# Performance work log

Hardware: AMD Instinct MI355X
Metric: run time of the kernel (lower is better)

## Reference

```python
import jax, jax.numpy as jnp
import numpy as np

# Architecture dims (from setArch args)
B, IN = 256, 1024          # batch, inputSize
E, H1, S = 32, 1024, 512   # numStateEnsembles, stateHiddenLayerSize, stateEnsembleOutputSize
H2, F = 512, 64            # featureHiddenLayerSize, numStateFeatures
NO, HO, OF = 16, 512, 1    # numOutputEnsembles, outputEnsembleHiddenLayerSize, outputEnsembleFeatures
T = E * F                  # thalamusSpaceSize
TIN = IN + T               # totalInputSize


def setup_inputs() -> dict:
    key = jax.random.key(0)
    ks = jax.random.split(key, 14)
    sc = 0.02
    f32 = jnp.float32
    return {
        "inputs": jax.random.normal(ks[0], (B, IN), f32),
        # stacked state-ensemble params: Linear(TIN,H1) -> Softplus -> Linear(H1,S)
        "sw1": jax.random.normal(ks[1], (E, TIN, H1), f32) * sc,
        "sb1": jax.random.normal(ks[2], (E, H1), f32) * sc,
        "sw2": jax.random.normal(ks[3], (E, H1, S), f32) * sc,
        "sb2": jax.random.normal(ks[4], (E, S), f32) * sc,
        # stacked feature-ensemble params: Linear(S,H2) -> ReLU -> Linear(H2,F)
        "fw1": jax.random.normal(ks[5], (E, S, H2), f32) * sc,
        "fb1": jax.random.normal(ks[6], (E, H2), f32) * sc,
        "fw2": jax.random.normal(ks[7], (E, H2, F), f32) * sc,
        "fb2": jax.random.normal(ks[8], (E, F), f32) * sc,
        # stacked output-ensemble params: Linear(S+1,HO) -> ReLU -> Linear(HO,OF)
        "ow1": jax.random.normal(ks[9], (NO, S + 1, HO), f32) * sc,
        "ob1": jax.random.normal(ks[10], (NO, HO), f32) * sc,
        "ow2": jax.random.normal(ks[11], (NO, HO, OF), f32) * sc,
        "ob2": jax.random.normal(ks[12], (NO, OF), f32) * sc,
        "action": 1,
        "context": 3,
        "num_iterations": 4,
    }


def reference(inputs, sw1, sb1, sw2, sb2, fw1, fb1, fw2, fb2,
              ow1, ob1, ow2, ob2, action, context, num_iterations):
    b = inputs.shape[0]
    # resetThalamus: savedThalamusFeatures = zeros(E*F)
    thal = jnp.zeros((b, T), inputs.dtype)
    state = None
    for _ in range(num_iterations):
        # leInput = cat(thalamusFeatures, inputs)  -> [B, TIN]
        x = jnp.concatenate([thal, inputs], axis=-1)
        # all E state ensembles batched: Linear -> Softplus -> Linear
        h = jax.nn.softplus(jnp.einsum('bi,eih->beh', x, sw1) + sb1)   # [B,E,H1]
        state = jnp.einsum('beh,ehs->bes', h, sw2) + sb2               # [B,E,S]
        # all E feature ensembles batched: Linear -> ReLU -> Linear
        g = jax.nn.relu(jnp.einsum('bes,esh->beh', state, fw1) + fb1)  # [B,E,H2]
        feat = jnp.einsum('beh,ehf->bef', g, fw2) + fb2                # [B,E,F]
        # thalamusFeatures = concatenate(computedFeatures)
        thal = feat.reshape(b, T)
    # output ensemble for `context` on cat([action], stateValues[context])
    sc_state = state[:, context, :]                                    # [B,S]
    a = jnp.full((b, 1), action, inputs.dtype)
    y = jnp.concatenate([a, sc_state], axis=-1)                        # [B,S+1]
    z = jax.nn.relu(y @ ow1[context] + ob1[context])                   # [B,HO]
    reward = z @ ow2[context] + ob2[context]                           # [B,OF]
    return reward
```

## Files before the change

### kernel.cpp

```cpp
#include <hip/hip_runtime.h>
#include <hip/hip_bf16.h>

#define B_SZ 256
#define IN_  1024
#define E_   32
#define H1_  1024
#define S_   512
#define H2_  512
#define F_   64
#define T_   2048
#define TIN_ 3072
#define NO_  16
#define HO_  512

typedef __attribute__((ext_vector_type(8))) short bf16x8;
typedef __attribute__((ext_vector_type(4))) float f32x4;

__device__ __forceinline__ unsigned short f2bf(float f) {
    unsigned u = __builtin_bit_cast(unsigned, f);
    u += 0x7fffu + ((u >> 16) & 1u);
    return (unsigned short)(u >> 16);
}
__device__ __forceinline__ float bf2f(unsigned short h) {
    return __builtin_bit_cast(float, ((unsigned)h) << 16);
}
__device__ __forceinline__ float softplusf(float x) {
    return fmaxf(x, 0.0f) + log1pf(expf(-fabsf(x)));
}
__device__ __forceinline__ void gload_lds16(const void* g, void* l) {
    __builtin_amdgcn_global_load_lds(
        (const __attribute__((address_space(1))) unsigned int*)g,
        (__attribute__((address_space(3))) unsigned int*)l,
        16, 0, 0);
}

__global__ __launch_bounds__(256) void cvt_t64(const float* __restrict__ in,
                                               unsigned short* __restrict__ out,
                                               int K, int N) {
    __shared__ float tile[64][65];
    const size_t eoff = (size_t)blockIdx.z * K * N;
    const float* ip = in + eoff;
    unsigned short* op = out + eoff;
    const int k0 = blockIdx.x * 64, n0 = blockIdx.y * 64;
    const int t = threadIdx.x;
    const int lr = t >> 4;
    const int lc = (t & 15) << 2;
    #pragma unroll
    for (int i = 0; i < 4; ++i) {
        const float4 v = *(const float4*)&ip[(size_t)(k0 + lr + 16 * i) * N + n0 + lc];
        float* dst = &tile[lr + 16 * i][lc];
        dst[0] = v.x; dst[1] = v.y; dst[2] = v.z; dst[3] = v.w;
    }
    __syncthreads();
    #pragma unroll
    for (int i = 0; i < 4; ++i) {
        const int n = (t >> 4) + 16 * i;
        const int k = (t & 15) << 2;
        ushort4 o;
        o.x = f2bf(tile[k][n]); o.y = f2bf(tile[k + 1][n]);
        o.z = f2bf(tile[k + 2][n]); o.w = f2bf(tile[k + 3][n]);
        *(ushort4*)&op[(size_t)(n0 + n) * K + k0 + k] = o;
    }
}

__global__ void x_init(const float* __restrict__ inp, unsigned short* __restrict__ x) {
    const int i = blockIdx.x * 256 + threadIdx.x;
    const int b = i / (IN_ / 4), c = (i % (IN_ / 4)) * 4;
    const float4 v = *(const float4*)&inp[(size_t)b * IN_ + c];
    ushort4 o;
    o.x = f2bf(v.x); o.y = f2bf(v.y); o.z = f2bf(v.z); o.w = f2bf(v.w);
    *(ushort4*)&x[(size_t)b * TIN_ + T_ + c] = o;
}

template<int BM, int BN, int TPB, int ACT, int ADD_BASE, int OUTM>
__global__ __launch_bounds__(TPB) void gemm_k(
    const unsigned short* __restrict__ A, int lda, long strideAe,
    int kOff, int K,
    const unsigned short* __restrict__ W, int ldw, long strideWe,
    const float* __restrict__ bias,
    const float* __restrict__ baseBuf,
    void* __restrict__ out, void* __restrict__ out2,
    int ldc, long strideOe, int N)
{
    constexpr int NW = TPB / 64;
    constexpr int WM_ = 2, WN_ = NW / 2;
    constexpr int MI = BM / (16 * WM_), NI = BN / (16 * WN_);
    constexpr int AL = (BM * 4) / TPB, BL = (BN * 4) / TPB;
    __shared__ unsigned short As0[BM * 32], Bs0[BN * 32];
    __shared__ unsigned short As1[BM * 32], Bs1[BN * 32];
    const int e = blockIdx.z;
    const int m0 = blockIdx.x * BM;
    const int n0 = blockIdx.y * BN;
    const int tid = threadIdx.x;
    const int wid = tid >> 6;
    const int lane = tid & 63;
    const int wm = wid / WN_, wn = wid % WN_;
    const unsigned short* Ae = A + (size_t)e * strideAe + (size_t)m0 * lda + kOff;
    const unsigned short* We = W + (size_t)e * strideWe + (size_t)n0 * ldw + kOff;

    f32x4 acc[MI][NI];
    #pragma unroll
    for (int i = 0; i < MI; ++i)
        #pragma unroll
        for (int j = 0; j < NI; ++j) {
            f32x4 z = {0.f, 0.f, 0.f, 0.f};
            acc[i][j] = z;
        }
    const int lr = lane & 15;
    const int lk = (lane >> 4) << 3;

    auto stage = [&](unsigned short* Asb, unsigned short* Bsb, int kt) {
        const int kk = kt * 32;
        #pragma unroll
        for (int p = 0; p < AL; ++p) {
            const int seg = p * TPB + tid;
            const int r = seg >> 2, cc = (seg & 3) << 3;
            gload_lds16(Ae + (size_t)r * lda + kk + cc, Asb + ((size_t)(p * TPB + wid * 64)) * 8);
        }
        #pragma unroll
        for (int p = 0; p < BL; ++p) {
            const int seg = p * TPB + tid;
            const int r = seg >> 2, cc = (seg & 3) << 3;
            gload_lds16(We + (size_t)r * ldw + kk + cc, Bsb + ((size_t)(p * TPB + wid * 64)) * 8);
        }
    };
    auto compute = [&](const unsigned short* Asb, const unsigned short* Bsb) {
        bf16x8 af2[MI], bfv[NI];
        #pragma unroll
        for (int mi = 0; mi < MI; ++mi)
            af2[mi] = *(const bf16x8*)&Asb[(wm * MI * 16 + mi * 16 + lr) * 32 + lk];
        #pragma unroll
        for (int ni = 0; ni < NI; ++ni)
            bfv[ni] = *(const bf16x8*)&Bsb[(wn * NI * 16 + ni * 16 + lr) * 32 + lk];
        #pragma unroll
        for (int mi = 0; mi < MI; ++mi)
            #pragma unroll
            for (int ni = 0; ni < NI; ++ni)
                acc[mi][ni] = __builtin_amdgcn_mfma_f32_16x16x32_bf16(
                    af2[mi], bfv[ni], acc[mi][ni], 0, 0, 0);
    };

    const int nt = K / 32;
    stage(As0, Bs0, 0);
    __syncthreads();
    for (int t = 0; t < nt; t += 2) {
        stage(As1, Bs1, t + 1);
        compute(As0, Bs0);
        __syncthreads();
        if (t + 2 < nt) stage(As0, Bs0, t + 2);
        compute(As1, Bs1);
        __syncthreads();
    }

    const int lg = lane >> 4;
    #pragma unroll
    for (int ni = 0; ni < NI; ++ni) {
        const int col = n0 + wn * NI * 16 + ni * 16 + lr;
        const float bv = bias ? bias[(size_t)e * N + col] : 0.0f;
        #pragma unroll
        for (int mi = 0; mi < MI; ++mi) {
            #pragma unroll
            for (int r = 0; r < 4; ++r) {
                const int row = m0 + wm * MI * 16 + mi * 16 + lg * 4 + r;
                float v = acc[mi][ni][r] + bv;
                if constexpr (ADD_BASE) v += baseBuf[((size_t)e * B_SZ + row) * H1_ + col];
                if constexpr (ACT == 1) v = softplusf(v);
                if constexpr (ACT == 2) v = fmaxf(v, 0.0f);
                const size_t oidx = (size_t)e * strideOe + (size_t)row * ldc + col;
                if constexpr (OUTM == 2) {
                    ((float*)out)[oidx] = v;
                    ((unsigned short*)out2)[oidx] = f2bf(softplusf(v));
                } else {
                    ((unsigned short*)out)[oidx] = f2bf(v);
                }
            }
        }
    }
    (void)out2;
}

__global__ __launch_bounds__(512) void head_z(const unsigned short* __restrict__ state,
                                              const float* __restrict__ ow1,
                                              const float* __restrict__ ob1,
                                              const int* __restrict__ actp,
                                              const int* __restrict__ ctxp,
                                              float* __restrict__ z) {
    __shared__ float ys[16][516];
    const int ctx = *ctxp;
    const float act = (float)(*actp);
    const int b0 = blockIdx.x * 16;
    const int t = threadIdx.x;
    for (int bb = 0; bb < 16; ++bb)
        ys[bb][1 + t] = bf2f(state[((size_t)(ctx * B_SZ + b0 + bb)) * S_ + t]);
    if (t < 16) ys[t][0] = act;
    __syncthreads();
    const float* w = ow1 + (size_t)ctx * (S_ + 1) * HO_;
    float acc[16];
    #pragma unroll
    for (int bb = 0; bb < 16; ++bb) acc[bb] = 0.0f;
    for (int k = 0; k < S_ + 1; ++k) {
        const float wv = w[(size_t)k * HO_ + t];
        #pragma unroll
        for (int bb = 0; bb < 16; ++bb) acc[bb] += ys[bb][k] * wv;
    }
    const float b1 = ob1[ctx * HO_ + t];
    for (int bb = 0; bb < 16; ++bb)
        z[(size_t)(b0 + bb) * HO_ + t] = fmaxf(acc[bb] + b1, 0.0f);
}

__global__ void head_r(const float* __restrict__ z, const float* __restrict__ ow2,
                       const float* __restrict__ ob2, const int* __restrict__ ctxp,
                       float* __restrict__ out) {
    const int ctx = *ctxp;
    const int b = blockIdx.x;
    const int t = threadIdx.x;
    const float* w = ow2 + (size_t)ctx * HO_;
    float s = 0.0f;
    for (int h = t; h < HO_; h += 64) s += z[(size_t)b * HO_ + h] * w[h];
    #pragma unroll
    for (int off = 32; off; off >>= 1) s += __shfl_down(s, off);
    if (t == 0) out[b] = s + ob2[ctx];
}

extern "C" void kernel_launch(void* const* d_in, const int* in_sizes, int n_in,
                              void* d_out, int out_size, void* d_ws, size_t ws_size,
                              hipStream_t stream) {
    (void)in_sizes; (void)n_in; (void)out_size; (void)ws_size;
    const float* inputs = (const float*)d_in[0];
    const float* sw1 = (const float*)d_in[1];
    const float* sb1 = (const float*)d_in[2];
    const float* sw2 = (const float*)d_in[3];
    const float* sb2 = (const float*)d_in[4];
    const float* fw1 = (const float*)d_in[5];
    const float* fb1 = (const float*)d_in[6];
    const float* fw2 = (const float*)d_in[7];
    const float* fb2 = (const float*)d_in[8];
    const float* ow1 = (const float*)d_in[9];
    const float* ob1 = (const float*)d_in[10];
    const float* ow2 = (const float*)d_in[11];
    const float* ob2 = (const float*)d_in[12];
    const int* actp = (const int*)d_in[13];
    const int* ctxp = (const int*)d_in[14];

    char* p = (char*)d_ws;
    unsigned short* w1t = (unsigned short*)p; p += (size_t)E_ * H1_ * TIN_ * 2;
    unsigned short* w2t = (unsigned short*)p; p += (size_t)E_ * S_ * H1_ * 2;
    unsigned short* f1t = (unsigned short*)p; p += (size_t)E_ * H2_ * S_ * 2;
    unsigned short* f2t = (unsigned short*)p; p += (size_t)E_ * F_ * H2_ * 2;
    unsigned short* xbf = (unsigned short*)p; p += (size_t)B_SZ * TIN_ * 2;
    float* base = (float*)p;                  p += (size_t)E_ * B_SZ * H1_ * 4;
    unsigned short* hbf = (unsigned short*)p; p += (size_t)E_ * B_SZ * H1_ * 2;
    unsigned short* stbf = (unsigned short*)p; p += (size_t)E_ * B_SZ * S_ * 2;
    unsigned short* gbf = (unsigned short*)p; p += (size_t)E_ * B_SZ * H2_ * 2;
    float* zbuf = (float*)p;                  p += (size_t)B_SZ * HO_ * 4;

    cvt_t64<<<dim3(TIN_ / 64, H1_ / 64, E_), 256, 0, stream>>>(sw1, w1t, TIN_, H1_);
    cvt_t64<<<dim3(H1_ / 64, S_ / 64, E_),  256, 0, stream>>>(sw2, w2t, H1_, S_);
    cvt_t64<<<dim3(S_ / 64, H2_ / 64, E_),  256, 0, stream>>>(fw1, f1t, S_, H2_);
    cvt_t64<<<dim3(H2_ / 64, F_ / 64, E_),  256, 0, stream>>>(fw2, f2t, H2_, F_);
    x_init<<<(B_SZ * IN_ / 4) / 256, 256, 0, stream>>>(inputs, xbf);

    gemm_k<128, 64, 256, 0, 0, 2><<<dim3(2, H1_ / 64, E_), 256, 0, stream>>>(
        xbf, TIN_, 0L, T_, IN_, w1t, TIN_, (long)H1_ * TIN_, sb1, nullptr,
        base, hbf, H1_, (long)B_SZ * H1_, H1_);

    for (int it = 0; it < 4; ++it) {
        if (it > 0) {
            gemm_k<128, 64, 256, 1, 1, 0><<<dim3(2, H1_ / 64, E_), 256, 0, stream>>>(
                xbf, TIN_, 0L, 0, T_, w1t, TIN_, (long)H1_ * TIN_, nullptr, base,
                hbf, nullptr, H1_, (long)B_SZ * H1_, H1_);
        }
        gemm_k<64, 64, 256, 0, 0, 0><<<dim3(4, S_ / 64, E_), 256, 0, stream>>>(
            hbf, H1_, (long)B_SZ * H1_, 0, H1_, w2t, H1_, (long)S_ * H1_, sb2, nullptr,
            stbf, nullptr, S_, (long)B_SZ * S_, S_);
        if (it < 3) {
            gemm_k<64, 64, 256, 2, 0, 0><<<dim3(4, H2_ / 64, E_), 256, 0, stream>>>(
                stbf, S_, (long)B_SZ * S_, 0, S_, f1t, S_, (long)H2_ * S_, fb1, nullptr,
                gbf, nullptr, H2_, (long)B_SZ * H2_, H2_);
            gemm_k<64, 64, 256, 0, 0, 0><<<dim3(4, 1, E_), 256, 0, stream>>>(
                gbf, H2_, (long)B_SZ * H2_, 0, H2_, f2t, H2_, (long)F_ * H2_, fb2, nullptr,
                xbf, nullptr, TIN_, 64L, F_);
        }
    }
    head_z<<<B_SZ / 16, 512, 0, stream>>>(stbf, ow1, ob1, actp, ctxp, zbuf);
    head_r<<<B_SZ, 64, 0, stream>>>(zbuf, ow2, ob2, ctxp, (float*)d_out);
}
```

Before: 880.9 us.

## Enlarge GEMM tiles, remap blocks M-major across ensembles, store base in bf16

Makes the warp layout a template parameter and moves the big first-layer GEMMs to 128x128 tiles with 512 threads. It also moves the second-layer and feature GEMMs to 128x64 tiles. A flat 1D grid ordered so that the two M-halves of the same weight tile are scheduled far apart (bid>>8) is meant to spread ensembles across CUs and keep the wave count even at 512 blocks. The precomputed input-part base activation is now stored in bf16 instead of fp32, halving its write and re-read traffic. The bf16 base adds rounding error to the pre-softplus sum.

```diff
diff --git a/kernel.cpp b/kernel.cpp
--- a/kernel.cpp
+++ b/kernel.cpp
@@ -72,29 +72,37 @@
     *(ushort4*)&x[(size_t)b * TIN_ + T_ + c] = o;
 }
 
-template<int BM, int BN, int TPB, int ACT, int ADD_BASE, int OUTM>
+template<int BM, int BN, int TPB, int WMT, int WNT, int ACT, int ADD_BASE, int OUTM, bool PAIRED>
 __global__ __launch_bounds__(TPB) void gemm_k(
     const unsigned short* __restrict__ A, int lda, long strideAe,
     int kOff, int K,
     const unsigned short* __restrict__ W, int ldw, long strideWe,
     const float* __restrict__ bias,
-    const float* __restrict__ baseBuf,
+    const unsigned short* __restrict__ baseBuf,
     void* __restrict__ out, void* __restrict__ out2,
     int ldc, long strideOe, int N)
 {
-    constexpr int NW = TPB / 64;
-    constexpr int WM_ = 2, WN_ = NW / 2;
-    constexpr int MI = BM / (16 * WM_), NI = BN / (16 * WN_);
+    constexpr int MI = BM / (16 * WMT), NI = BN / (16 * WNT);
     constexpr int AL = (BM * 4) / TPB, BL = (BN * 4) / TPB;
     __shared__ unsigned short As0[BM * 32], Bs0[BN * 32];
     __shared__ unsigned short As1[BM * 32], Bs1[BN * 32];
-    const int e = blockIdx.z;
-    const int m0 = blockIdx.x * BM;
-    const int n0 = blockIdx.y * BN;
+
+    int e, m0, n0;
+    if constexpr (PAIRED) {
+        const int bid = blockIdx.x;
+        const int NBn = N / BN;
+        m0 = (bid >> 8) * BM;
+        const int rem = bid & 255;
+        n0 = (rem % NBn) * BN;
+        e  = rem / NBn;
+    } else {
+        e = blockIdx.z; m0 = blockIdx.x * BM; n0 = blockIdx.y * BN;
+    }
+
     const int tid = threadIdx.x;
     const int wid = tid >> 6;
     const int lane = tid & 63;
-    const int wm = wid / WN_, wn = wid % WN_;
+    const int wm = wid / WNT, wn = wid % WNT;
     const unsigned short* Ae = A + (size_t)e * strideAe + (size_t)m0 * lda + kOff;
     const unsigned short* We = W + (size_t)e * strideWe + (size_t)n0 * ldw + kOff;
 
@@ -163,12 +171,12 @@
             for (int r = 0; r < 4; ++r) {
                 const int row = m0 + wm * MI * 16 + mi * 16 + lg * 4 + r;
                 float v = acc[mi][ni][r] + bv;
-                if constexpr (ADD_BASE) v += baseBuf[((size_t)e * B_SZ + row) * H1_ + col];
+                if constexpr (ADD_BASE) v += bf2f(baseBuf[((size_t)e * B_SZ + row) * H1_ + col]);
                 if constexpr (ACT == 1) v = softplusf(v);
                 if constexpr (ACT == 2) v = fmaxf(v, 0.0f);
                 const size_t oidx = (size_t)e * strideOe + (size_t)row * ldc + col;
                 if constexpr (OUTM == 2) {
-                    ((float*)out)[oidx] = v;
+                    ((unsigned short*)out)[oidx] = f2bf(v);
                     ((unsigned short*)out2)[oidx] = f2bf(softplusf(v));
                 } else {
                     ((unsigned short*)out)[oidx] = f2bf(v);
@@ -248,7 +256,7 @@
     unsigned short* f1t = (unsigned short*)p; p += (size_t)E_ * H2_ * S_ * 2;
     unsigned short* f2t = (unsigned short*)p; p += (size_t)E_ * F_ * H2_ * 2;
     unsigned short* xbf = (unsigned short*)p; p += (size_t)B_SZ * TIN_ * 2;
-    float* base = (float*)p;                  p += (size_t)E_ * B_SZ * H1_ * 4;
+    unsigned short* base = (unsigned short*)p; p += (size_t)E_ * B_SZ * H1_ * 2;
     unsigned short* hbf = (unsigned short*)p; p += (size_t)E_ * B_SZ * H1_ * 2;
     unsigned short* stbf = (unsigned short*)p; p += (size_t)E_ * B_SZ * S_ * 2;
     unsigned short* gbf = (unsigned short*)p; p += (size_t)E_ * B_SZ * H2_ * 2;
@@ -260,24 +268,24 @@
     cvt_t64<<<dim3(H2_ / 64, F_ / 64, E_),  256, 0, stream>>>(fw2, f2t, H2_, F_);
     x_init<<<(B_SZ * IN_ / 4) / 256, 256, 0, stream>>>(inputs, xbf);
 
-    gemm_k<128, 64, 256, 0, 0, 2><<<dim3(2, H1_ / 64, E_), 256, 0, stream>>>(
+    gemm_k<128, 128, 512, 2, 4, 0, 0, 2, true><<<dim3(512), 512, 0, stream>>>(
         xbf, TIN_, 0L, T_, IN_, w1t, TIN_, (long)H1_ * TIN_, sb1, nullptr,
         base, hbf, H1_, (long)B_SZ * H1_, H1_);
 
     for (int it = 0; it < 4; ++it) {
         if (it > 0) {
-            gemm_k<128, 64, 256, 1, 1, 0><<<dim3(2, H1_ / 64, E_), 256, 0, stream>>>(
+            gemm_k<128, 128, 512, 2, 4, 1, 1, 0, true><<<dim3(512), 512, 0, stream>>>(
                 xbf, TIN_, 0L, 0, T_, w1t, TIN_, (long)H1_ * TIN_, nullptr, base,
                 hbf, nullptr, H1_, (long)B_SZ * H1_, H1_);
         }
-        gemm_k<64, 64, 256, 0, 0, 0><<<dim3(4, S_ / 64, E_), 256, 0, stream>>>(
+        gemm_k<128, 64, 256, 2, 2, 0, 0, 0, true><<<dim3(512), 256, 0, stream>>>(
             hbf, H1_, (long)B_SZ * H1_, 0, H1_, w2t, H1_, (long)S_ * H1_, sb2, nullptr,
             stbf, nullptr, S_, (long)B_SZ * S_, S_);
         if (it < 3) {
-            gemm_k<64, 64, 256, 2, 0, 0><<<dim3(4, H2_ / 64, E_), 256, 0, stream>>>(
+            gemm_k<128, 64, 256, 2, 2, 2, 0, 0, true><<<dim3(512), 256, 0, stream>>>(
                 stbf, S_, (long)B_SZ * S_, 0, S_, f1t, S_, (long)H2_ * S_, fb1, nullptr,
                 gbf, nullptr, H2_, (long)B_SZ * H2_, H2_);
-            gemm_k<64, 64, 256, 0, 0, 0><<<dim3(4, 1, E_), 256, 0, stream>>>(
+            gemm_k<64, 64, 256, 2, 2, 0, 0, 0, false><<<dim3(4, 1, E_), 256, 0, stream>>>(
                 gbf, H2_, (long)B_SZ * H2_, 0, H2_, f2t, H2_, (long)F_ * H2_, fb2, nullptr,
                 xbf, nullptr, TIN_, 64L, F_);
         }
```

Result: faster. 744.5 us, median of 2 (-15.5%).
